# Performance work log

Measured on AMD Instinct MI355X. Metric: run time of the kernel, lower is better.

## Reference

```python
import jax, jax.numpy as jnp
import numpy as np

BATCH = 512
MODES = 256
WIDTH = 256  # modes == width required by the `x @ weights[1]` contraction


def crelu(z):
    # torch.relu is undefined on complex; the evident intent is componentwise relu
    return jax.nn.relu(z.real) + 1j * jax.nn.relu(z.imag)


def setup_inputs() -> dict:
    key = jax.random.key(0)
    ks = jax.random.split(key, 7)
    x = jax.random.normal(ks[0], (BATCH, MODES), dtype=jnp.float32)
    w0 = jax.random.normal(ks[1], (MODES, WIDTH), dtype=jnp.float32)
    w1 = jax.random.normal(ks[2], (MODES, WIDTH), dtype=jnp.float32)
    s = 1.0 / np.sqrt(WIDTH)
    lin1_w = jax.random.uniform(ks[3], (WIDTH, WIDTH), jnp.float32, -s, s)
    lin1_b = jax.random.uniform(ks[4], (WIDTH,), jnp.float32, -s, s)
    lin2_w = jax.random.uniform(ks[5], (WIDTH, WIDTH), jnp.float32, -s, s)
    lin2_b = jax.random.uniform(ks[6], (WIDTH,), jnp.float32, -s, s)
    return {"x": x, "w0": w0, "w1": w1,
            "lin1_w": lin1_w, "lin1_b": lin1_b,
            "lin2_w": lin2_w, "lin2_b": lin2_b}


def reference(x, w0, w1, lin1_w, lin1_b, lin2_w, lin2_b):
    modes = w0.shape[0]
    # torch.fft.fftn defaults to all dims
    X = jnp.fft.fftn(x)                                   # (B, modes) complex64
    # mode-wise lift: x.unsqueeze(-1) (*) weights[0]
    h = X[..., None] * w0                                 # (B, modes, width)
    h = crelu(h)
    # L = diag(exp(i 2pi n / modes)); dense L @ h == diagonal elementwise multiply
    phase = jnp.exp(1j * (2.0 * np.pi / modes)
                    * jnp.arange(modes, dtype=jnp.float32))  # (modes,) complex64
    h = phase[:, None] * h                                # (B, modes, width)
    # x @ weights[1]: contracts h's width dim with weights[1]'s first dim (modes==width)
    h = jnp.einsum('bmw,wv->bmv', h, w1.astype(h.dtype))  # (B, modes, width)
    h = h @ lin1_w.T.astype(h.dtype) + lin1_b             # Linear(width, width)
    h = crelu(h)
    h = h @ lin2_w.T.astype(h.dtype) + lin2_b             # Linear(width, width)
    return jnp.fft.ifftn(h)                               # (B, modes, width) complex64
```

## Files before the change

### kernel.cpp

```cpp
#include <hip/hip_runtime.h>
#include <hip/hip_bf16.h>


typedef unsigned short ushort_t;
typedef unsigned int   uint_t;
typedef __attribute__((ext_vector_type(8))) short short8b;
typedef __attribute__((ext_vector_type(4))) float f32x4;

__device__ __forceinline__ uint_t packf2(float lo, float hi){
  union { __hip_bfloat162 h; uint_t u; } v;
  v.h = __float22bfloat162_rn(make_float2(lo, hi));
  return v.u;
}
__device__ __forceinline__ ushort_t f2bf(float f){
  union { __hip_bfloat16 h; ushort_t u; } v;
  v.h = __float2bfloat16(f);
  return v.u;
}
__device__ __forceinline__ float bf_lo(uint_t u){
  union { uint_t u; float f; } v; v.u = u << 16; return v.f;
}
__device__ __forceinline__ float bf_hi(uint_t u){
  union { uint_t u; float f; } v; v.u = u & 0xFFFF0000u; return v.f;
}
__device__ __forceinline__ void gld16(const void* g, void* l){
  __builtin_amdgcn_global_load_lds(
      (const __attribute__((address_space(1))) void*)g,
      (__attribute__((address_space(3))) void*)l, 16, 0, 0);
}

constexpr int BR16T[16] = {0,8,4,12,2,10,6,14,1,9,5,13,3,11,7,15};
constexpr int BR32T[32] = {0,16,8,24,4,20,12,28,2,18,10,26,6,22,14,30,
                           1,17,9,25,5,21,13,29,3,19,11,27,7,23,15,31};

__device__ __forceinline__ void bfly(float& ar, float& ai, float& br, float& bi,
                                     float wr, float wi){
  float sr = ar - br, si = ai - bi;
  ar += br; ai += bi;
  br = sr*wr - si*wi;
  bi = sr*wi + si*wr;
}

__device__ __forceinline__ void fft16_inv(float* xr, float* xi){
  const float C1 = 0.92387953251128674f, S1 = 0.38268343236508978f,
              C2 = 0.70710678118654752f;
  bfly(xr[0],xi[0],xr[8],xi[8],    1.f, 0.f);
  bfly(xr[1],xi[1],xr[9],xi[9],    C1,  S1);
  bfly(xr[2],xi[2],xr[10],xi[10],  C2,  C2);
  bfly(xr[3],xi[3],xr[11],xi[11],  S1,  C1);
  bfly(xr[4],xi[4],xr[12],xi[12],  0.f, 1.f);
  bfly(xr[5],xi[5],xr[13],xi[13], -S1,  C1);
  bfly(xr[6],xi[6],xr[14],xi[14], -C2,  C2);
  bfly(xr[7],xi[7],xr[15],xi[15], -C1,  S1);
  #pragma unroll
  for (int h = 0; h < 16; h += 8){
    bfly(xr[h+0],xi[h+0],xr[h+4],xi[h+4],  1.f, 0.f);
    bfly(xr[h+1],xi[h+1],xr[h+5],xi[h+5],  C2,  C2);
    bfly(xr[h+2],xi[h+2],xr[h+6],xi[h+6],  0.f, 1.f);
    bfly(xr[h+3],xi[h+3],xr[h+7],xi[h+7], -C2,  C2);
  }
  #pragma unroll
  for (int h = 0; h < 16; h += 4){
    bfly(xr[h+0],xi[h+0],xr[h+2],xi[h+2], 1.f, 0.f);
    bfly(xr[h+1],xi[h+1],xr[h+3],xi[h+3], 0.f, 1.f);
  }
  #pragma unroll
  for (int h = 0; h < 16; h += 2)
    bfly(xr[h],xi[h],xr[h+1],xi[h+1], 1.f, 0.f);
}

__device__ __forceinline__ void fft32_inv(float* xr, float* xi){
  constexpr float WR[16] = {
    1.f, 0.98078528040323044f, 0.92387953251128674f, 0.83146961230254524f,
    0.70710678118654752f, 0.55557023301960222f, 0.38268343236508978f, 0.19509032201612827f,
    0.f,-0.19509032201612827f,-0.38268343236508978f,-0.55557023301960222f,
   -0.70710678118654752f,-0.83146961230254524f,-0.92387953251128674f,-0.98078528040323044f};
  constexpr float WI[16] = {
    0.f, 0.19509032201612827f, 0.38268343236508978f, 0.55557023301960222f,
    0.70710678118654752f, 0.83146961230254524f, 0.92387953251128674f, 0.98078528040323044f,
    1.f, 0.98078528040323044f, 0.92387953251128674f, 0.83146961230254524f,
    0.70710678118654752f, 0.55557023301960222f, 0.38268343236508978f, 0.19509032201612827f};
  #pragma unroll
  for (int j = 0; j < 16; ++j)
    bfly(xr[j],xi[j],xr[j+16],xi[j+16], WR[j], WI[j]);
  fft16_inv(xr, xi);
  fft16_inv(xr+16, xi+16);
}

__global__ void fill_tables(float2* t256f, float2* t256i, float2* t512f, float2* t512i){
  int i = threadIdx.x;
  const double PI2 = 6.283185307179586476925286766559;
  if (i < 256){
    double a = PI2 * (double)i / 256.0;
    float c = (float)cos(a), s = (float)sin(a);
    t256f[i] = make_float2(c, -s);
    t256i[i] = make_float2(c,  s);
  }
  {
    double a = PI2 * (double)i / 512.0;
    float c = (float)cos(a), s = (float)sin(a);
    t512f[i] = make_float2(c, -s);
    t512i[i] = make_float2(c,  s);
  }
}

__global__ void dft_m(const float* __restrict__ x, float2* __restrict__ Yw,
                      const float2* __restrict__ twf){
  __shared__ float xs[256];
  __shared__ float2 tws[256];
  int b = blockIdx.x, k = threadIdx.x;
  xs[k]  = x[b*256 + k];
  tws[k] = twf[k];
  __syncthreads();
  float yr = 0.f, yi = 0.f;
  for (int m = 0; m < 256; ++m){
    float2 w = tws[(m*k) & 255];
    float xv = xs[m];
    yr += xv*w.x; yi += xv*w.y;
  }
  Yw[b*256 + k] = make_float2(yr, yi);
}

__global__ void dft_b(const float2* __restrict__ Yw, float* __restrict__ Xr,
                      float* __restrict__ Xi, const float2* __restrict__ twf){
  __shared__ float2 tws[512];
  int j = blockIdx.x, k = threadIdx.x;
  tws[k]       = twf[k];
  tws[k + 256] = twf[k + 256];
  __syncthreads();
  float xr = 0.f, xi = 0.f;
  for (int b = 0; b < 512; ++b){
    float2 y = Yw[b*256 + k];
    float2 w = tws[(b*j) & 511];
    xr += y.x*w.x - y.y*w.y;
    xi += y.x*w.y + y.y*w.x;
  }
  Xr[j*256 + k] = xr;
  Xi[j*256 + k] = xi;
}

__global__ void prep_w(const float* __restrict__ w1, const float* __restrict__ lin1_w,
                       const float* __restrict__ lin2_w,
                       ushort_t* __restrict__ Wct, ushort_t* __restrict__ W2b){
  __shared__ float l1[256];
  int u = blockIdx.x, t = threadIdx.x;
  l1[t] = lin1_w[u*256 + t];
  __syncthreads();
  float s = 0.f;
  for (int v = 0; v < 256; ++v)
    s += l1[v] * w1[t*256 + v];
  Wct[u*256 + t] = f2bf(s);
  W2b[u*256 + t] = f2bf(lin2_w[u*256 + t]);
}

#define ZJS 300

__global__ __launch_bounds__(512, 4)
void fused_mid(const float* __restrict__ Xr, const float* __restrict__ Xi,
               const float* __restrict__ w0,
               const ushort_t* __restrict__ Wct, const ushort_t* __restrict__ W2b,
               const float* __restrict__ b1, const float* __restrict__ b2,
               const float2* __restrict__ ph,
               uint_t* __restrict__ OutP)
{
  __shared__ __align__(16) char lds[65536];
  ushort_t* H3 = (ushort_t*)(lds + 32768);
  uint_t*   Z  = (uint_t*)lds;

  const int tid  = threadIdx.x;
  const int lane = tid & 63;
  const int w8   = tid >> 6;
  const int L    = lane & 15;
  const int chk  = lane >> 4;
  const int cq   = chk, cl = L;
  const int cr0  = blockIdx.x * 32;

  const int arow = tid >> 3;
  const int ak0  = (tid & 7) * 4;
  const int ajj  = arow & 31;
  const bool aim = arow >= 32;
  const float axr = Xr[cr0 + ajj];
  const float axi = Xi[cr0 + ajj];
  const float2 apj = ph[(cr0 + ajj) & 255];
  const int am = (cr0 + ajj) & 255;
  const int aslot = (ak0 >> 3) ^ ((arow >> 1) & 3);
  const int aoff  = arow*64 + aslot*16 + (ak0 & 7)*2;

  const int fsl  = chk ^ ((L >> 1) & 3);
  const int avix = L*32 + fsl*8;
  const int bvix = w8*1024 + avix;

  const int bc = (tid & 3) ^ ((tid >> 3) & 3);

  f32x4 acc[4][2];
  #pragma unroll
  for (int m = 0; m < 4; ++m)
    #pragma unroll
    for (int n = 0; n < 2; ++n)
      acc[m][n] = (f32x4){0.f,0.f,0.f,0.f};

  #define STAGE_B(W, kt, bsel) do {                                        \
    char* _d = lds + (bsel)*16384 + tid*16;                                \
    _Pragma("unroll")                                                      \
    for (int _i = 0; _i < 2; ++_i){                                        \
      int _row = _i*128 + (tid >> 2);                                      \
      gld16((W) + _row*256 + (kt)*32 + bc*8, _d + _i*8192);                \
    }                                                                      \
  } while(0)

  #define STAGE_A(kt, bsel) do {                                           \
    const float4 _w4 = *(const float4*)&w0[(size_t)am*256 + (kt)*32 + ak0];\
    float _wv[4] = {_w4.x, _w4.y, _w4.z, _w4.w};                           \
    float _va[4];                                                          \
    _Pragma("unroll")                                                      \
    for (int _e = 0; _e < 4; ++_e){                                        \
      float _r = fmaxf(axr*_wv[_e], 0.f);                                  \
      float _m = fmaxf(axi*_wv[_e], 0.f);                                  \
      _va[_e] = aim ? (apj.y*_r + apj.x*_m) : (apj.x*_r - apj.y*_m);       \
    }                                                                      \
    *(uint2*)(lds + 32768 + (bsel)*4096 + aoff) =                          \
        make_uint2(packf2(_va[0], _va[1]), packf2(_va[2], _va[3]));        \
  } while(0)

  int buf = 0;
  STAGE_B(Wct, 0, 0);
  STAGE_A(0, 0);
  __syncthreads();
  for (int kt = 0; kt < 8; ++kt){
    if (kt < 7){ STAGE_B(Wct, kt+1, buf^1); STAGE_A(kt+1, buf^1); }
    const ushort_t* Ab = (const ushort_t*)(lds + 32768 + buf*4096);
    const ushort_t* Bb = (const ushort_t*)(lds + buf*16384);
    short8b av[4], bv[2];
    #pragma unroll
    for (int m = 0; m < 4; ++m) av[m] = *(const short8b*)&Ab[avix + m*512];
    #pragma unroll
    for (int n = 0; n < 2; ++n) bv[n] = *(const short8b*)&Bb[bvix + n*512];
    #pragma unroll
    for (int m = 0; m < 4; ++m)
      #pragma unroll
      for (int n = 0; n < 2; ++n)
        acc[m][n] = __builtin_amdgcn_mfma_f32_16x16x32_bf16(av[m], bv[n], acc[m][n], 0,0,0);
    __syncthreads();
    buf ^= 1;
  }

  STAGE_B(W2b, 0, 0);
  #pragma unroll
  for (int m = 0; m < 4; ++m){
    #pragma unroll
    for (int n = 0; n < 2; ++n){
      int col = w8*32 + n*16 + cl;
      float badd = (m < 2) ? b1[col] : 0.f;
      #pragma unroll
      for (int q = 0; q < 4; ++q){
        int row = m*16 + cq*4 + q;
        float v = fmaxf(acc[m][n][q] + badd, 0.f);
        int s = (col >> 3) ^ (row & 7);
        H3[row*256 + s*8 + (col & 7)] = f2bf(v);
      }
    }
  }
  __syncthreads();

  #pragma unroll
  for (int m = 0; m < 4; ++m)
    #pragma unroll
    for (int n = 0; n < 2; ++n)
      acc[m][n] = (f32x4){0.f,0.f,0.f,0.f};

  buf = 0;
  for (int kt = 0; kt < 8; ++kt){
    if (kt < 7) STAGE_B(W2b, kt+1, buf^1);
    const ushort_t* Bb = (const ushort_t*)(lds + buf*16384);
    short8b av[4], bv[2];
    #pragma unroll
    for (int m = 0; m < 4; ++m){
      int r = m*16 + L;
      int s = (kt*4 + chk) ^ (r & 7);
      av[m] = *(const short8b*)&H3[r*256 + s*8];
    }
    #pragma unroll
    for (int n = 0; n < 2; ++n) bv[n] = *(const short8b*)&Bb[bvix + n*512];
    #pragma unroll
    for (int m = 0; m < 4; ++m)
      #pragma unroll
      for (int n = 0; n < 2; ++n)
        acc[m][n] = __builtin_amdgcn_mfma_f32_16x16x32_bf16(av[m], bv[n], acc[m][n], 0,0,0);
    __syncthreads();
    buf ^= 1;
  }

  #pragma unroll
  for (int m2 = 0; m2 < 2; ++m2){
    #pragma unroll
    for (int n = 0; n < 2; ++n){
      int col = w8*32 + n*16 + cl;
      float bias2 = b2[col];
      int a = col >> 4;
      #pragma unroll
      for (int q = 0; q < 4; ++q){
        int j = m2*16 + cq*4 + q;
        Z[j*ZJS + a*16 + cl] = packf2(acc[m2][n][q] + bias2, acc[m2+2][n][q]);
      }
    }
  }
  __syncthreads();

  {
    const int j1 = tid >> 4;
    const int b1c = tid & 15;
    float sr[16], si[16];
    #pragma unroll
    for (int a = 0; a < 16; ++a){
      uint_t u = Z[j1*ZJS + a*16 + b1c];
      sr[a] = bf_lo(u); si[a] = bf_hi(u);
    }
    fft16_inv(sr, si);
    float2 ws = ph[b1c];
    float wr = 1.f/256.f, wi = 0.f;
    #pragma unroll
    for (int d = 0; d < 16; ++d){
      float yr = sr[BR16T[d]], yi = si[BR16T[d]];
      Z[j1*ZJS + d*16 + b1c] = packf2(yr*wr - yi*wi, yr*wi + yi*wr);
      float nw = wr*ws.x - wi*ws.y;
      wi = wr*ws.y + wi*ws.x; wr = nw;
    }
  }
  __syncthreads();

  {
    const int j2 = tid >> 4;
    const int d2 = tid & 15;
    float br[16], bi[16];
    const uint4* zb = (const uint4*)&Z[j2*ZJS + d2*16];
    #pragma unroll
    for (int c = 0; c < 4; ++c){
      uint4 u4 = zb[c];
      br[c*4+0] = bf_lo(u4.x); bi[c*4+0] = bf_hi(u4.x);
      br[c*4+1] = bf_lo(u4.y); bi[c*4+1] = bf_hi(u4.y);
      br[c*4+2] = bf_lo(u4.z); bi[c*4+2] = bf_hi(u4.z);
      br[c*4+3] = bf_lo(u4.w); bi[c*4+3] = bf_hi(u4.w);
    }
    fft16_inv(br, bi);
    const long rowbase = (long)(cr0 + j2) * 256;
    #pragma unroll
    for (int p = 0; p < 16; ++p)
      OutP[rowbase + BR16T[p]*16 + d2] = packf2(br[p], bi[p]);
  }
  #undef STAGE_B
  #undef STAGE_A
}

__global__ __launch_bounds__(256)
void fft_m(uint_t* __restrict__ P, const float2* __restrict__ ph){
  __shared__ uint_t Z[4352];
  const int tid = threadIdx.x;
  const int v = tid & 15;
  const int b = tid >> 4;
  const int bB = blockIdx.x >> 4;
  const int vg = (blockIdx.x & 15) << 4;
  const long base = (long)bB*65536 + vg + v;

  float xr[16], xi[16];
  #pragma unroll
  for (int a = 0; a < 16; ++a){
    uint_t u = P[base + (long)(a*16 + b)*256];
    xr[a] = bf_lo(u); xi[a] = bf_hi(u);
  }
  fft16_inv(xr, xi);
  float2 ws = ph[b];
  float wr = 1.f/256.f, wi = 0.f;
  #pragma unroll
  for (int d = 0; d < 16; ++d){
    float yr = xr[BR16T[d]], yi = xi[BR16T[d]];
    Z[d*272 + b*17 + v] = packf2(yr*wr - yi*wi, yr*wi + yi*wr);
    float nw = wr*ws.x - wi*ws.y; wi = wr*ws.y + wi*ws.x; wr = nw;
  }
  __syncthreads();
  const int d2 = tid >> 4;
  float br[16], bi[16];
  #pragma unroll
  for (int bb = 0; bb < 16; ++bb){
    uint_t u = Z[d2*272 + bb*17 + v];
    br[bb] = bf_lo(u); bi[bb] = bf_hi(u);
  }
  fft16_inv(br, bi);
  #pragma unroll
  for (int p = 0; p < 16; ++p)
    P[base + (long)(BR16T[p]*16 + d2)*256] = packf2(br[p], bi[p]);
}

__global__ __launch_bounds__(256)
void fft_b(uint_t* __restrict__ P, const float2* __restrict__ t512){
  __shared__ uint_t Z[8704];
  const int tid = threadIdx.x;
  const int v = tid & 15;
  const int b = tid >> 4;
  const int m = blockIdx.x >> 4;
  const int vg = (blockIdx.x & 15) << 4;
  const long base = (long)m*256 + vg + v;

  float xr[32], xi[32];
  #pragma unroll
  for (int a = 0; a < 32; ++a){
    uint_t u = P[base + (long)(a*16 + b)*65536];
    xr[a] = bf_lo(u); xi[a] = bf_hi(u);
  }
  fft32_inv(xr, xi);
  float2 ws = t512[b];
  float wr = 1.f/512.f, wi = 0.f;
  #pragma unroll
  for (int d = 0; d < 32; ++d){
    float yr = xr[BR32T[d]], yi = xi[BR32T[d]];
    Z[d*272 + b*17 + v] = packf2(yr*wr - yi*wi, yr*wi + yi*wr);
    float nw = wr*ws.x - wi*ws.y; wi = wr*ws.y + wi*ws.x; wr = nw;
  }
  __syncthreads();
  float* out = (float*)P;
  #pragma unroll
  for (int h = 0; h < 2; ++h){
    const int d = (tid >> 4) + 16*h;
    float br[16], bi[16];
    #pragma unroll
    for (int bb = 0; bb < 16; ++bb){
      uint_t u = Z[d*272 + bb*17 + v];
      br[bb] = bf_lo(u); bi[bb] = bf_hi(u);
    }
    fft16_inv(br, bi);
    #pragma unroll
    for (int p = 0; p < 16; ++p)
      out[base + (long)(BR16T[p]*32 + d)*65536] = br[p];
  }
}

extern "C" void kernel_launch(void* const* d_in, const int* in_sizes, int n_in,
                              void* d_out, int out_size, void* d_ws, size_t ws_size,
                              hipStream_t stream) {
  (void)in_sizes; (void)n_in; (void)out_size; (void)ws_size;
  const float* x      = (const float*)d_in[0];
  const float* w0     = (const float*)d_in[1];
  const float* w1     = (const float*)d_in[2];
  const float* lin1_w = (const float*)d_in[3];
  const float* lin1_b = (const float*)d_in[4];
  const float* lin2_w = (const float*)d_in[5];
  const float* lin2_b = (const float*)d_in[6];

  char* sm = (char*)d_ws;
  float2*   Yw     = (float2*)sm;   sm += 1048576;
  float*    Xr     = (float*)sm;    sm += 524288;
  float*    Xi     = (float*)sm;    sm += 524288;
  float2*   t256f  = (float2*)sm;   sm += 2048;
  float2*   t256i  = (float2*)sm;   sm += 2048;
  float2*   t512f  = (float2*)sm;   sm += 4096;
  float2*   t512i  = (float2*)sm;   sm += 4096;
  ushort_t* Wct    = (ushort_t*)sm; sm += 131072;
  ushort_t* W2b    = (ushort_t*)sm; sm += 131072;

  uint_t* planes = (uint_t*)d_out;

  fill_tables<<<1, 512, 0, stream>>>(t256f, t256i, t512f, t512i);
  dft_m<<<512, 256, 0, stream>>>(x, Yw, t256f);
  dft_b<<<512, 256, 0, stream>>>(Yw, Xr, Xi, t512f);
  prep_w<<<256, 256, 0, stream>>>(w1, lin1_w, lin2_w, Wct, W2b);
  fused_mid<<<4096, 512, 0, stream>>>(Xr, Xi, w0, Wct, W2b, lin1_b, lin2_b,
                                      t256i, planes);
  fft_m<<<8192, 256, 0, stream>>>(planes, t256i);
  fft_b<<<4096, 256, 0, stream>>>(planes, t512i);
}
```

Measured before the change: 320.3 us.

## Fold width-axis inverse DFT into lin2 weights and widen FFT blocks

Precomputes a complex matrix that combines lin2 with the inverse DFT along the width axis (and a matching transformed bias). The second GEMM in fused_mid becomes a complex GEMM producing already-transformed output, which removes the in-kernel radix-16 FFT passes and the LDS staging they needed. The cost is doubling the second GEMM's MFMA work and weight traffic. Separately, fft_m and fft_b now use 512-thread blocks covering 32 columns with unpadded LDS rows, halving the grid size.

```diff
diff --git a/kernel.cpp b/kernel.cpp
--- a/kernel.cpp
+++ b/kernel.cpp
@@ -140,8 +140,7 @@
 }
 
 __global__ void prep_w(const float* __restrict__ w1, const float* __restrict__ lin1_w,
-                       const float* __restrict__ lin2_w,
-                       ushort_t* __restrict__ Wct, ushort_t* __restrict__ W2b){
+                       ushort_t* __restrict__ Wct){
   __shared__ float l1[256];
   int u = blockIdx.x, t = threadIdx.x;
   l1[t] = lin1_w[u*256 + t];
@@ -150,22 +149,44 @@
   for (int v = 0; v < 256; ++v)
     s += l1[v] * w1[t*256 + v];
   Wct[u*256 + t] = f2bf(s);
-  W2b[u*256 + t] = f2bf(lin2_w[u*256 + t]);
-}
-
-#define ZJS 300
+}
+
+__global__ void prep_g(const float* __restrict__ lin2_w, const float2* __restrict__ ph,
+                       ushort_t* __restrict__ BtR, ushort_t* __restrict__ BtI){
+  int v = blockIdx.x, k = threadIdx.x;
+  float cre = 0.f, cim = 0.f;
+  for (int u = 0; u < 256; ++u){
+    float w = lin2_w[u*256 + k];
+    float2 t = ph[(u*v) & 255];
+    cre += w*t.x; cim += w*t.y;
+  }
+  BtR[v*256 + k] = f2bf(cre * (1.f/256.f));
+  BtI[v*256 + k] = f2bf(cim * (1.f/256.f));
+}
+
+__global__ void prep_b2g(const float* __restrict__ b2, const float2* __restrict__ ph,
+                         float2* __restrict__ b2g){
+  int v = threadIdx.x;
+  float cre = 0.f, cim = 0.f;
+  for (int u = 0; u < 256; ++u){
+    float w = b2[u];
+    float2 t = ph[(u*v) & 255];
+    cre += w*t.x; cim += w*t.y;
+  }
+  b2g[v] = make_float2(cre * (1.f/256.f), cim * (1.f/256.f));
+}
 
 __global__ __launch_bounds__(512, 4)
 void fused_mid(const float* __restrict__ Xr, const float* __restrict__ Xi,
                const float* __restrict__ w0,
-               const ushort_t* __restrict__ Wct, const ushort_t* __restrict__ W2b,
-               const float* __restrict__ b1, const float* __restrict__ b2,
+               const ushort_t* __restrict__ Wct,
+               const ushort_t* __restrict__ BtR, const ushort_t* __restrict__ BtI,
+               const float* __restrict__ b1, const float2* __restrict__ b2g,
                const float2* __restrict__ ph,
                uint_t* __restrict__ OutP)
 {
   __shared__ __align__(16) char lds[65536];
   ushort_t* H3 = (ushort_t*)(lds + 32768);
-  uint_t*   Z  = (uint_t*)lds;
 
   const int tid  = threadIdx.x;
   const int lane = tid & 63;
@@ -191,13 +212,6 @@
   const int bvix = w8*1024 + avix;
 
   const int bc = (tid & 3) ^ ((tid >> 3) & 3);
-
-  f32x4 acc[4][2];
-  #pragma unroll
-  for (int m = 0; m < 4; ++m)
-    #pragma unroll
-    for (int n = 0; n < 2; ++n)
-      acc[m][n] = (f32x4){0.f,0.f,0.f,0.f};
 
   #define STAGE_B(W, kt, bsel) do {                                        \
     char* _d = lds + (bsel)*16384 + tid*16;                                \
@@ -222,6 +236,13 @@
         make_uint2(packf2(_va[0], _va[1]), packf2(_va[2], _va[3]));        \
   } while(0)
 
+  f32x4 acc[4][2];
+  #pragma unroll
+  for (int m = 0; m < 4; ++m)
+    #pragma unroll
+    for (int n = 0; n < 2; ++n)
+      acc[m][n] = (f32x4){0.f,0.f,0.f,0.f};
+
   int buf = 0;
   STAGE_B(Wct, 0, 0);
   STAGE_A(0, 0);
@@ -244,7 +265,7 @@
     buf ^= 1;
   }
 
-  STAGE_B(W2b, 0, 0);
+  STAGE_B(BtR, 0, 0);
   #pragma unroll
   for (int m = 0; m < 4; ++m){
     #pragma unroll
@@ -262,126 +283,102 @@
   }
   __syncthreads();
 
+  f32x4 accR[4][2], accI[4][2];
   #pragma unroll
   for (int m = 0; m < 4; ++m)
     #pragma unroll
-    for (int n = 0; n < 2; ++n)
-      acc[m][n] = (f32x4){0.f,0.f,0.f,0.f};
+    for (int n = 0; n < 2; ++n){
+      accR[m][n] = (f32x4){0.f,0.f,0.f,0.f};
+      accI[m][n] = (f32x4){0.f,0.f,0.f,0.f};
+    }
 
   buf = 0;
-  for (int kt = 0; kt < 8; ++kt){
-    if (kt < 7) STAGE_B(W2b, kt+1, buf^1);
-    const ushort_t* Bb = (const ushort_t*)(lds + buf*16384);
+  for (int kp = 0; kp < 8; ++kp){
     short8b av[4], bv[2];
     #pragma unroll
     for (int m = 0; m < 4; ++m){
       int r = m*16 + L;
-      int s = (kt*4 + chk) ^ (r & 7);
-      av[m] = *(const short8b*)&H3[r*256 + s*8];
-    }
-    #pragma unroll
-    for (int n = 0; n < 2; ++n) bv[n] = *(const short8b*)&Bb[bvix + n*512];
-    #pragma unroll
-    for (int m = 0; m < 4; ++m)
-      #pragma unroll
-      for (int n = 0; n < 2; ++n)
-        acc[m][n] = __builtin_amdgcn_mfma_f32_16x16x32_bf16(av[m], bv[n], acc[m][n], 0,0,0);
+      int sl = (kp*4 + chk) ^ (r & 7);
+      av[m] = *(const short8b*)&H3[r*256 + sl*8];
+    }
+    STAGE_B(BtI, kp, buf^1);
+    {
+      const ushort_t* Bb = (const ushort_t*)(lds + buf*16384);
+      #pragma unroll
+      for (int n = 0; n < 2; ++n) bv[n] = *(const short8b*)&Bb[bvix + n*512];
+      #pragma unroll
+      for (int m = 0; m < 4; ++m)
+        #pragma unroll
+        for (int n = 0; n < 2; ++n)
+          accR[m][n] = __builtin_amdgcn_mfma_f32_16x16x32_bf16(av[m], bv[n], accR[m][n], 0,0,0);
+    }
     __syncthreads();
     buf ^= 1;
-  }
-
-  #pragma unroll
-  for (int m2 = 0; m2 < 2; ++m2){
-    #pragma unroll
-    for (int n = 0; n < 2; ++n){
-      int col = w8*32 + n*16 + cl;
-      float bias2 = b2[col];
-      int a = col >> 4;
+    if (kp < 7) STAGE_B(BtR, kp+1, buf^1);
+    {
+      const ushort_t* Bb = (const ushort_t*)(lds + buf*16384);
+      #pragma unroll
+      for (int n = 0; n < 2; ++n) bv[n] = *(const short8b*)&Bb[bvix + n*512];
+      #pragma unroll
+      for (int m = 0; m < 4; ++m)
+        #pragma unroll
+        for (int n = 0; n < 2; ++n)
+          accI[m][n] = __builtin_amdgcn_mfma_f32_16x16x32_bf16(av[m], bv[n], accI[m][n], 0,0,0);
+    }
+    __syncthreads();
+    buf ^= 1;
+  }
+
+  #pragma unroll
+  for (int n = 0; n < 2; ++n){
+    int col = w8*32 + n*16 + cl;
+    float2 bg = b2g[col];
+    #pragma unroll
+    for (int m2 = 0; m2 < 2; ++m2){
       #pragma unroll
       for (int q = 0; q < 4; ++q){
         int j = m2*16 + cq*4 + q;
-        Z[j*ZJS + a*16 + cl] = packf2(acc[m2][n][q] + bias2, acc[m2+2][n][q]);
+        float vr = accR[m2][n][q]   - accI[m2+2][n][q] + bg.x;
+        float vi = accI[m2][n][q]   + accR[m2+2][n][q] + bg.y;
+        OutP[(long)(cr0 + j)*256 + col] = packf2(vr, vi);
       }
     }
-  }
-  __syncthreads();
-
-  {
-    const int j1 = tid >> 4;
-    const int b1c = tid & 15;
-    float sr[16], si[16];
-    #pragma unroll
-    for (int a = 0; a < 16; ++a){
-      uint_t u = Z[j1*ZJS + a*16 + b1c];
-      sr[a] = bf_lo(u); si[a] = bf_hi(u);
-    }
-    fft16_inv(sr, si);
-    float2 ws = ph[b1c];
-    float wr = 1.f/256.f, wi = 0.f;
-    #pragma unroll
-    for (int d = 0; d < 16; ++d){
-      float yr = sr[BR16T[d]], yi = si[BR16T[d]];
-      Z[j1*ZJS + d*16 + b1c] = packf2(yr*wr - yi*wi, yr*wi + yi*wr);
-      float nw = wr*ws.x - wi*ws.y;
-      wi = wr*ws.y + wi*ws.x; wr = nw;
-    }
-  }
-  __syncthreads();
-
-  {
-    const int j2 = tid >> 4;
-    const int d2 = tid & 15;
-    float br[16], bi[16];
-    const uint4* zb = (const uint4*)&Z[j2*ZJS + d2*16];
-    #pragma unroll
-    for (int c = 0; c < 4; ++c){
-      uint4 u4 = zb[c];
-      br[c*4+0] = bf_lo(u4.x); bi[c*4+0] = bf_hi(u4.x);
-      br[c*4+1] = bf_lo(u4.y); bi[c*4+1] = bf_hi(u4.y);
-      br[c*4+2] = bf_lo(u4.z); bi[c*4+2] = bf_hi(u4.z);
-      br[c*4+3] = bf_lo(u4.w); bi[c*4+3] = bf_hi(u4.w);
-    }
-    fft16_inv(br, bi);
-    const long rowbase = (long)(cr0 + j2) * 256;
-    #pragma unroll
-    for (int p = 0; p < 16; ++p)
-      OutP[rowbase + BR16T[p]*16 + d2] = packf2(br[p], bi[p]);
   }
   #undef STAGE_B
   #undef STAGE_A
 }
 
-__global__ __launch_bounds__(256)
+__global__ __launch_bounds__(512)
 void fft_m(uint_t* __restrict__ P, const float2* __restrict__ ph){
-  __shared__ uint_t Z[4352];
+  __shared__ uint_t Z[8192];
   const int tid = threadIdx.x;
-  const int v = tid & 15;
-  const int b = tid >> 4;
-  const int bB = blockIdx.x >> 4;
-  const int vg = (blockIdx.x & 15) << 4;
+  const int v  = tid & 31;
+  const int bm = tid >> 5;
+  const int bB = blockIdx.x >> 3;
+  const int vg = (blockIdx.x & 7) << 5;
   const long base = (long)bB*65536 + vg + v;
 
   float xr[16], xi[16];
   #pragma unroll
   for (int a = 0; a < 16; ++a){
-    uint_t u = P[base + (long)(a*16 + b)*256];
+    uint_t u = P[base + (long)(a*16 + bm)*256];
     xr[a] = bf_lo(u); xi[a] = bf_hi(u);
   }
   fft16_inv(xr, xi);
-  float2 ws = ph[b];
+  float2 ws = ph[bm];
   float wr = 1.f/256.f, wi = 0.f;
   #pragma unroll
   for (int d = 0; d < 16; ++d){
     float yr = xr[BR16T[d]], yi = xi[BR16T[d]];
-    Z[d*272 + b*17 + v] = packf2(yr*wr - yi*wi, yr*wi + yi*wr);
+    Z[d*512 + bm*32 + v] = packf2(yr*wr - yi*wi, yr*wi + yi*wr);
     float nw = wr*ws.x - wi*ws.y; wi = wr*ws.y + wi*ws.x; wr = nw;
   }
   __syncthreads();
-  const int d2 = tid >> 4;
+  const int d2 = tid >> 5;
   float br[16], bi[16];
   #pragma unroll
   for (int bb = 0; bb < 16; ++bb){
-    uint_t u = Z[d2*272 + bb*17 + v];
+    uint_t u = Z[d2*512 + bb*32 + v];
     br[bb] = bf_lo(u); bi[bb] = bf_hi(u);
   }
   fft16_inv(br, bi);
@@ -390,40 +387,40 @@
     P[base + (long)(BR16T[p]*16 + d2)*256] = packf2(br[p], bi[p]);
 }
 
-__global__ __launch_bounds__(256)
+__global__ __launch_bounds__(512)
 void fft_b(uint_t* __restrict__ P, const float2* __restrict__ t512){
-  __shared__ uint_t Z[8704];
+  __shared__ uint_t Z[16384];
   const int tid = threadIdx.x;
-  const int v = tid & 15;
-  const int b = tid >> 4;
-  const int m = blockIdx.x >> 4;
-  const int vg = (blockIdx.x & 15) << 4;
+  const int v  = tid & 31;
+  const int bq = tid >> 5;
+  const int m  = blockIdx.x >> 3;
+  const int vg = (blockIdx.x & 7) << 5;
   const long base = (long)m*256 + vg + v;
 
   float xr[32], xi[32];
   #pragma unroll
   for (int a = 0; a < 32; ++a){
-    uint_t u = P[base + (long)(a*16 + b)*65536];
+    uint_t u = P[base + (long)(a*16 + bq)*65536];
     xr[a] = bf_lo(u); xi[a] = bf_hi(u);
   }
   fft32_inv(xr, xi);
-  float2 ws = t512[b];
+  float2 ws = t512[bq];
   float wr = 1.f/512.f, wi = 0.f;
   #pragma unroll
   for (int d = 0; d < 32; ++d){
     float yr = xr[BR32T[d]], yi = xi[BR32T[d]];
-    Z[d*272 + b*17 + v] = packf2(yr*wr - yi*wi, yr*wi + yi*wr);
+    Z[d*512 + bq*32 + v] = packf2(yr*wr - yi*wi, yr*wi + yi*wr);
     float nw = wr*ws.x - wi*ws.y; wi = wr*ws.y + wi*ws.x; wr = nw;
   }
   __syncthreads();
   float* out = (float*)P;
   #pragma unroll
   for (int h = 0; h < 2; ++h){
-    const int d = (tid >> 4) + 16*h;
+    const int d = (tid >> 5) + 16*h;
     float br[16], bi[16];
     #pragma unroll
     for (int bb = 0; bb < 16; ++bb){
-      uint_t u = Z[d*272 + bb*17 + v];
+      uint_t u = Z[d*512 + bb*32 + v];
       br[bb] = bf_lo(u); bi[bb] = bf_hi(u);
     }
     fft16_inv(br, bi);
@@ -454,16 +451,20 @@
   float2*   t512f  = (float2*)sm;   sm += 4096;
   float2*   t512i  = (float2*)sm;   sm += 4096;
   ushort_t* Wct    = (ushort_t*)sm; sm += 131072;
-  ushort_t* W2b    = (ushort_t*)sm; sm += 131072;
+  ushort_t* BtR    = (ushort_t*)sm; sm += 131072;
+  ushort_t* BtI    = (ushort_t*)sm; sm += 131072;
+  float2*   b2g    = (float2*)sm;   sm += 2048;
 
   uint_t* planes = (uint_t*)d_out;
 
   fill_tables<<<1, 512, 0, stream>>>(t256f, t256i, t512f, t512i);
   dft_m<<<512, 256, 0, stream>>>(x, Yw, t256f);
   dft_b<<<512, 256, 0, stream>>>(Yw, Xr, Xi, t512f);
-  prep_w<<<256, 256, 0, stream>>>(w1, lin1_w, lin2_w, Wct, W2b);
-  fused_mid<<<4096, 512, 0, stream>>>(Xr, Xi, w0, Wct, W2b, lin1_b, lin2_b,
+  prep_w<<<256, 256, 0, stream>>>(w1, lin1_w, Wct);
+  prep_g<<<256, 256, 0, stream>>>(lin2_w, t256i, BtR, BtI);
+  prep_b2g<<<1, 256, 0, stream>>>(lin2_b, t256i, b2g);
+  fused_mid<<<4096, 512, 0, stream>>>(Xr, Xi, w0, Wct, BtR, BtI, lin1_b, b2g,
                                       t256i, planes);
-  fft_m<<<8192, 256, 0, stream>>>(planes, t256i);
-  fft_b<<<4096, 256, 0, stream>>>(planes, t512i);
-}
+  fft_m<<<4096, 512, 0, stream>>>(planes, t256i);
+  fft_b<<<2048, 512, 0, stream>>>(planes, t512i);
+}
```

New measurement: 327.5 us. 2.2% more time.
